# Kernel optimization log

Hardware: AMD Instinct MI355X
Metric: run time of the kernel (lower is better)

The kernel has to match this reference:

```python
import jax, jax.numpy as jnp
import numpy as np

B, T, S, G, D, H, W, CHUNK = 2, 4096, 4096, 64, 1024, 16, 512, 256
HD = D // H


def setup_inputs() -> dict:
    key = jax.random.key(0)
    ks = jax.random.split(key, 16)
    std = 1.0 / np.sqrt(D)
    w = lambda k: jax.random.normal(k, (D, D), jnp.float32) * std
    b = lambda k: jax.random.normal(k, (D,), jnp.float32) * 0.01
    return {
        "query": jax.random.normal(ks[0], (B, T, D), jnp.float32),
        "encoder_out": jax.random.normal(ks[1], (B, S, D), jnp.float32),
        "global_tokens": jax.random.normal(ks[2], (B, G, D), jnp.float32),
        "qw": w(ks[3]), "qb": b(ks[4]),
        "kw": w(ks[5]), "kb": b(ks[6]),
        "vw": w(ks[7]), "vb": b(ks[8]),
        "gkw": w(ks[9]), "gkb": b(ks[10]),
        "gvw": w(ks[11]), "gvb": b(ks[12]),
        "ow": w(ks[13]), "ob": b(ks[14]),
        "compression_ratio": 1,
    }


def reference(query, encoder_out, global_tokens, qw, qb, kw, kb, vw, vb,
              gkw, gkb, gvw, gvb, ow, ob, compression_ratio):
    scale = jnp.float32(np.sqrt(HD))
    r = jnp.float32(compression_ratio)
    # expected raw position for each decoder step, clamped to valid src range
    expected = jnp.clip((jnp.arange(T, dtype=jnp.float32) / r).astype(jnp.int32), 0, S - 1)
    expected = jnp.broadcast_to(expected[None], (B, T))  # [B,T]

    lin = lambda x, wt, bs: x @ wt.T + bs  # torch nn.Linear: y = x W^T + b
    q = lin(query, qw, qb).reshape(B, T, H, HD).transpose(0, 2, 1, 3)            # [B,H,T,HD]
    gk = lin(global_tokens, gkw, gkb).reshape(B, G, H, HD).transpose(0, 2, 1, 3)  # [B,H,G,HD]
    gv = lin(global_tokens, gvw, gvb).reshape(B, G, H, HD).transpose(0, 2, 1, 3)
    ak = lin(encoder_out, kw, kb).reshape(B, S, H, HD).transpose(0, 2, 1, 3)      # [B,H,S,HD]
    av = lin(encoder_out, vw, vb).reshape(B, S, H, HD).transpose(0, 2, 1, 3)

    nC = T // CHUNK
    # per-(batch,chunk) window start, from the middle query's expected position
    centers = expected.reshape(B, nC, CHUNK)[:, :, CHUNK // 2]   # [B,nC]
    win_start = jnp.clip(centers - W // 2, 0, S - W)             # [B,nC]; window always full length W
    idx = win_start[:, :, None] + jnp.arange(W)[None, None, :]   # [B,nC,W]

    gather = lambda kv_b, idx_b: kv_b[:, idx_b, :]               # [H,S,HD],[nC,W] -> [H,nC,W,HD]
    wk = jax.vmap(gather)(ak, idx)                               # [B,H,nC,W,HD]
    wv = jax.vmap(gather)(av, idx)

    qc = q.reshape(B, H, nC, CHUNK, HD)
    sg = jnp.einsum('bhcqd,bhgd->bhcqg', qc, gk) / scale          # global scores  [B,H,nC,CHUNK,G]
    sl = jnp.einsum('bhcqd,bhcwd->bhcqw', qc, wk) / scale         # windowed scores [B,H,nC,CHUNK,W]
    attn = jax.nn.softmax(jnp.concatenate([sg, sl], axis=-1), axis=-1)
    out = (jnp.einsum('bhcqg,bhgd->bhcqd', attn[..., :G], gv)
           + jnp.einsum('bhcqw,bhcwd->bhcqd', attn[..., G:], wv))  # [B,H,nC,CHUNK,HD]
    out = out.reshape(B, H, T, HD).transpose(0, 2, 1, 3).reshape(B, T, D)
    return lin(out, ow, ob)
```

## Files before the change

kernel.cpp:

```cpp
#include <hip/hip_runtime.h>

typedef unsigned short u16;
typedef unsigned int u32;
typedef __attribute__((ext_vector_type(4))) float f32x4;
typedef __attribute__((ext_vector_type(16))) float f32x16;
typedef __attribute__((ext_vector_type(8))) short bf16x8;

constexpr int B_ = 2, T_ = 4096, S_ = 4096, G_ = 64, D_ = 1024, H_ = 16, W_ = 512, CHUNK_ = 256;
constexpr int NC_ = T_ / CHUNK_;
constexpr int NT_ = (G_ + W_) / 32;

__device__ __forceinline__ u16 f2bf(float x) {
  u32 u = __builtin_bit_cast(u32, x);
  return (u16)((u + 0x7FFFu + ((u >> 16) & 1u)) >> 16);
}

__global__ __launch_bounds__(256) void cvt_all_kernel(const float* __restrict__ q, const float* __restrict__ e,
                                                      const float* __restrict__ g, const float* __restrict__ w0,
                                                      const float* __restrict__ w1, const float* __restrict__ w2,
                                                      const float* __restrict__ w3, const float* __restrict__ w4,
                                                      const float* __restrict__ w5, u16* __restrict__ dst) {
  int blk = blockIdx.x;
  const float* src;
  int sblk;
  if (blk < 8192) { src = q; sblk = 0; }
  else if (blk < 16384) { src = e; sblk = 8192; }
  else if (blk < 16512) { src = g; sblk = 16384; }
  else if (blk < 17536) { src = w0; sblk = 16512; }
  else if (blk < 18560) { src = w1; sblk = 17536; }
  else if (blk < 19584) { src = w2; sblk = 18560; }
  else if (blk < 20608) { src = w3; sblk = 19584; }
  else if (blk < 21632) { src = w4; sblk = 20608; }
  else { src = w5; sblk = 21632; }
  int li = (blk - sblk) * 256 + threadIdx.x;
  size_t gi = (size_t)blk * 256 + threadIdx.x;
  float4 v = ((const float4*)src)[li];
  uint2 o;
  o.x = (u32)f2bf(v.x) | ((u32)f2bf(v.y) << 16);
  o.y = (u32)f2bf(v.z) | ((u32)f2bf(v.w) << 16);
  ((uint2*)dst)[gi] = o;
}

__global__ __launch_bounds__(256, 2) void proj_kernel(const u16* __restrict__ ex, const u16* __restrict__ qx,
                                                      const u16* __restrict__ gx, const u16* __restrict__ wgt,
                                                      const float* __restrict__ qb, const float* __restrict__ kbias,
                                                      const float* __restrict__ vbias, const float* __restrict__ gkb,
                                                      const float* __restrict__ gvb, u16* __restrict__ q_bf,
                                                      u16* __restrict__ k_bf, u16* __restrict__ gk_bf) {
  __shared__ char lds[73728];
  constexpr size_t NW = (size_t)D_ * D_;
  constexpr size_t NQs = (size_t)B_ * T_ * D_;
  constexpr size_t NGs = (size_t)B_ * G_ * D_;
  const int tid = threadIdx.x;
  const int lane = tid & 63;
  const int wid = tid >> 6;
  const int wm = wid >> 1, wn = wid & 1;
  const int l15 = lane & 15, kg = lane >> 4;

  const int bid = blockIdx.x;
  const u16 *A, *Bt;
  const float *b1, *b2;
  u16* out;
  int row0, col0, mloc;
  bool scale = false, dual = false;
  size_t dsplit = 0;
  if (bid < 512) {
    row0 = (bid & 31) * 256; col0 = (bid >> 5) * 128; mloc = 256;
    A = ex; Bt = wgt + NW; b1 = kbias; b2 = vbias; out = k_bf; dsplit = NQs; dual = true;
  } else if (bid < 768) {
    int i = bid - 512;
    row0 = (i & 31) * 256; col0 = (i >> 5) * 128; mloc = 256;
    A = qx; Bt = wgt; b1 = qb; b2 = qb; out = q_bf; scale = true;
  } else {
    int i = bid - 768;
    row0 = 0; col0 = i * 128; mloc = 128;
    A = gx; Bt = wgt + 3 * NW; b1 = gkb; b2 = gvb; out = gk_bf; dsplit = NGs; dual = true;
  }
  const float* bp = b1;
  u16* op = out;
  if (dual && col0 >= 1024) { bp = b2 - 1024; op = out + (dsplit - 1024); }

  f32x4 acc[8][4];
#pragma unroll
  for (int i = 0; i < 8; i++)
#pragma unroll
    for (int j = 0; j < 4; j++)
#pragma unroll
      for (int r = 0; r < 4; r++) acc[i][j][r] = 0.f;

  const char* Abase = (const char*)A;
  const char* Bbase = (const char*)Bt;
  const int swb = 16 * ((tid & 3) ^ ((tid >> 3) & 3));

  auto stageA = [&](int slot, int kt) {
#pragma unroll
    for (int p = 0; p < 4; p++) {
      int dst = slot * 16384 + p * 4096 + tid * 16;
      const char* g = Abase + (size_t)(row0 + p * 64 + (tid >> 2)) * 2048 + kt * 64 + swb;
      __builtin_amdgcn_global_load_lds((const __attribute__((address_space(1))) void*)g,
                                       (__attribute__((address_space(3))) void*)(lds + dst), 16, 0, 0);
    }
  };
  auto stageB = [&](int slot, int kt) {
#pragma unroll
    for (int p = 0; p < 2; p++) {
      int dst = 49152 + slot * 8192 + p * 4096 + tid * 16;
      const char* g = Bbase + (size_t)(col0 + p * 64 + (tid >> 2)) * 2048 + kt * 64 + swb;
      __builtin_amdgcn_global_load_lds((const __attribute__((address_space(1))) void*)g,
                                       (__attribute__((address_space(3))) void*)(lds + dst), 16, 0, 0);
    }
  };

  stageA(0, 0); stageB(0, 0);
  stageA(1, 1); stageB(1, 1);
  asm volatile("s_waitcnt vmcnt(6)" ::: "memory");
  __builtin_amdgcn_s_barrier();

  int cur = 0, nx = 2;
  for (int t = 0; t < 32; ++t) {
    const char* Ab = lds + cur * 16384;
    const char* Bb = lds + 49152 + cur * 8192;
    bf16x8 bfv[2], af[4];
#pragma unroll
    for (int ni = 0; ni < 2; ni++) {
      int r = wn * 64 + ni * 16 + l15;
      (void)r;
    }
    bf16x8 bq[4];
#pragma unroll
    for (int ni = 0; ni < 4; ni++) {
      int r = wn * 64 + ni * 16 + l15;
      bq[ni] = *(const bf16x8*)(Bb + ((r * 64 + kg * 16) ^ (((r >> 1) & 3) << 4)));
    }
#pragma unroll
    for (int mi = 0; mi < 4; mi++) {
      int r = wm * 128 + mi * 16 + l15;
      af[mi] = *(const bf16x8*)(Ab + ((r * 64 + kg * 16) ^ (((r >> 1) & 3) << 4)));
    }
    if (t + 2 < 32) stageA(nx, t + 2);
    __builtin_amdgcn_s_barrier();
    __builtin_amdgcn_s_setprio(1);
#pragma unroll
    for (int mi = 0; mi < 4; mi++)
#pragma unroll
      for (int ni = 0; ni < 4; ni++)
        acc[mi][ni] = __builtin_amdgcn_mfma_f32_16x16x32_bf16(bq[ni], af[mi], acc[mi][ni], 0, 0, 0);
    __builtin_amdgcn_s_setprio(0);
    __builtin_amdgcn_s_barrier();
#pragma unroll
    for (int mi = 0; mi < 4; mi++) {
      int r = wm * 128 + (mi + 4) * 16 + l15;
      af[mi] = *(const bf16x8*)(Ab + ((r * 64 + kg * 16) ^ (((r >> 1) & 3) << 4)));
    }
    if (t + 2 < 32) stageB(nx, t + 2);
    __builtin_amdgcn_s_barrier();
    __builtin_amdgcn_s_setprio(1);
#pragma unroll
    for (int mi = 0; mi < 4; mi++)
#pragma unroll
      for (int ni = 0; ni < 4; ni++)
        acc[mi + 4][ni] = __builtin_amdgcn_mfma_f32_16x16x32_bf16(bq[ni], af[mi], acc[mi + 4][ni], 0, 0, 0);
    __builtin_amdgcn_s_setprio(0);
    if (t < 30) {
      asm volatile("s_waitcnt vmcnt(6)" ::: "memory");
    } else if (t == 30) {
      asm volatile("s_waitcnt vmcnt(0)" ::: "memory");
    }
    __builtin_amdgcn_s_barrier();
    cur = cur == 2 ? 0 : cur + 1;
    nx = nx == 2 ? 0 : nx + 1;
  }

  float4 bv4[4];
#pragma unroll
  for (int ni = 0; ni < 4; ni++) bv4[ni] = *(const float4*)&bp[col0 + wn * 64 + ni * 16 + kg * 4];
#pragma unroll
  for (int mi = 0; mi < 8; mi++) {
    int rloc = wm * 128 + mi * 16 + l15;
    if (rloc >= mloc) continue;
    size_t grow = (size_t)(row0 + rloc);
#pragma unroll
    for (int ni = 0; ni < 4; ni++) {
      int gcol = col0 + wn * 64 + ni * 16 + kg * 4;
      float v0 = acc[mi][ni][0] + bv4[ni].x;
      float v1 = acc[mi][ni][1] + bv4[ni].y;
      float v2 = acc[mi][ni][2] + bv4[ni].z;
      float v3 = acc[mi][ni][3] + bv4[ni].w;
      if (scale) {
        v0 *= 0.18033688011112042f; v1 *= 0.18033688011112042f;
        v2 *= 0.18033688011112042f; v3 *= 0.18033688011112042f;
      }
      uint2 o;
      asm("v_cvt_pk_bf16_f32 %0, %1, %2" : "=v"(o.x) : "v"(v0), "v"(v1));
      asm("v_cvt_pk_bf16_f32 %0, %1, %2" : "=v"(o.y) : "v"(v2), "v"(v3));
      *(uint2*)&op[grow * 1024 + gcol] = o;
    }
  }
}

template <int MODE>
__global__ __launch_bounds__(256) void gemm_kernel(const u16* __restrict__ A, const u16* __restrict__ Bt,
                                                   const float* __restrict__ bias, const float* __restrict__ bias2,
                                                   size_t split, void* __restrict__ out) {
  __shared__ char lds[32768];
  char* As = lds;
  char* Bs = lds + 16384;
  const int tid = threadIdx.x;
  const int lane = tid & 63;
  const int wv = tid >> 6;
  const int wr = wv >> 1, wc = wv & 1;
  const int l15 = lane & 15, kg = lane >> 4;
  const int row0 = blockIdx.x * 128;
  const int col0 = blockIdx.y * 128;

  f32x4 acc[4][4];
#pragma unroll
  for (int i = 0; i < 4; i++)
#pragma unroll
    for (int j = 0; j < 4; j++)
#pragma unroll
      for (int r = 0; r < 4; r++) acc[i][j][r] = 0.f;

  const char* Abase = (const char*)A;
  const char* Bbase = (const char*)Bt;

  const int kb = 16 * ((lane & 3) ^ ((lane >> 3) & 3));
  auto stage = [&](int bufsel, int k0) {
#pragma unroll
    for (int c = 0; c < 2; c++) {
      int arow = wv * 32 + c * 16 + (lane >> 2);
      int dsto = bufsel * 8192 + wv * 2048 + c * 1024 + lane * 16;
      const char* ga = Abase + ((size_t)(row0 + arow) * 2048 + (size_t)k0 * 2 + kb);
      __builtin_amdgcn_global_load_lds((const __attribute__((address_space(1))) void*)ga,
                                       (__attribute__((address_space(3))) void*)(As + dsto), 16, 0, 0);
      const char* gb = Bbase + ((size_t)(col0 + arow) * 2048 + (size_t)k0 * 2 + kb);
      __builtin_amdgcn_global_load_lds((const __attribute__((address_space(1))) void*)gb,
                                       (__attribute__((address_space(3))) void*)(Bs + dsto), 16, 0, 0);
    }
  };

  stage(0, 0);
  __syncthreads();

  for (int it = 0; it < 32; ++it) {
    const int cur = it & 1;
    if (it + 1 < 32) stage(cur ^ 1, (it + 1) * 32);

    const char* Ab = As + cur * 8192;
    const char* Bb = Bs + cur * 8192;
    bf16x8 af[4], bfv[4];
#pragma unroll
    for (int mi = 0; mi < 4; mi++) {
      int row = wr * 64 + mi * 16 + l15;
      af[mi] = *(const bf16x8*)(Ab + ((row * 64 + kg * 16) ^ ((row & 6) << 3)));
    }
#pragma unroll
    for (int ni = 0; ni < 4; ni++) {
      int row = wc * 64 + ni * 16 + l15;
      bfv[ni] = *(const bf16x8*)(Bb + ((row * 64 + kg * 16) ^ ((row & 6) << 3)));
    }
    __builtin_amdgcn_s_setprio(1);
#pragma unroll
    for (int mi = 0; mi < 4; mi++)
#pragma unroll
      for (int ni = 0; ni < 4; ni++)
        acc[mi][ni] = __builtin_amdgcn_mfma_f32_16x16x32_bf16(bfv[ni], af[mi], acc[mi][ni], 0, 0, 0);
    __builtin_amdgcn_s_setprio(0);
    __syncthreads();
  }

  const float* bp = bias;
  (void)bias2; (void)split;
  float4 bv4[4];
#pragma unroll
  for (int ni = 0; ni < 4; ni++) bv4[ni] = *(const float4*)&bp[col0 + wc * 64 + ni * 16 + kg * 4];
#pragma unroll
  for (int mi = 0; mi < 4; mi++) {
    size_t grow = (size_t)(row0 + wr * 64 + mi * 16 + l15);
#pragma unroll
    for (int ni = 0; ni < 4; ni++) {
      int gcol = col0 + wc * 64 + ni * 16 + kg * 4;
      float v0 = acc[mi][ni][0] + bv4[ni].x;
      float v1 = acc[mi][ni][1] + bv4[ni].y;
      float v2 = acc[mi][ni][2] + bv4[ni].z;
      float v3 = acc[mi][ni][3] + bv4[ni].w;
      if (MODE == 2) {
        float4 fo = {v0, v1, v2, v3};
        *(float4*)&((float*)out)[grow * 1024 + gcol] = fo;
      } else {
        uint2 o;
        asm("v_cvt_pk_bf16_f32 %0, %1, %2" : "=v"(o.x) : "v"(v0), "v"(v1));
        asm("v_cvt_pk_bf16_f32 %0, %1, %2" : "=v"(o.y) : "v"(v2), "v"(v3));
        *(uint2*)&((u16*)out)[grow * 1024 + gcol] = o;
      }
    }
  }
}

__global__ __launch_bounds__(512, 4) void attn_kernel(const u16* __restrict__ q_bf, const u16* __restrict__ k_bf,
                                                      const u16* __restrict__ v_bf, const u16* __restrict__ gk_bf,
                                                      const u16* __restrict__ gv_bf, u16* __restrict__ ao,
                                                      const int* __restrict__ rptr) {
  __shared__ u16 smem[16384];
  const int c = blockIdx.x, h = blockIdx.y, b = blockIdx.z;
  const int tid = threadIdx.x;
  const int lane = tid & 63, wv = tid >> 6;
  const int l31 = lane & 31, half = lane >> 5;
  const int t0 = c * CHUNK_;

  int rr = rptr[0];
  int centert = c * CHUNK_ + CHUNK_ / 2;
  int expected = (int)((float)centert / (float)rr);
  expected = min(max(expected, 0), S_ - 1);
  int ws0 = min(max(expected - W_ / 2, 0), S_ - W_);

  bf16x8 qf[4];
  {
    const u16* qrow = q_bf + ((size_t)(b * T_ + t0 + wv * 32 + l31)) * D_ + h * 64 + half * 8;
#pragma unroll
    for (int s = 0; s < 4; s++) qf[s] = *(const bf16x8*)(qrow + s * 16);
  }

  const int skey = (tid & 255) >> 3, shq = tid & 7;
  const bool isK = tid < 256;

  auto load_tile = [&](int j) -> uint4 {
    const u16* base;
    size_t row;
    if (j < 2) {
      base = isK ? gk_bf : gv_bf;
      row = (size_t)(b * G_ + j * 32 + skey);
    } else {
      base = isK ? k_bf : v_bf;
      row = (size_t)(b * S_ + ws0 + (j - 2) * 32 + skey);
    }
    return *(const uint4*)(base + row * D_ + h * 64 + shq * 8);
  };

  f32x16 oacc[2];
#pragma unroll
  for (int i = 0; i < 2; i++)
#pragma unroll
    for (int r = 0; r < 16; r++) oacc[i][r] = 0.f;
  float mrun = -1e30f, lsum = 0.f;

  uint4 stg = load_tile(0);

  for (int j = 0; j < NT_; j++) {
    const int bsel = j & 1;
    if (isK) {
      *(uint4*)((char*)smem + bsel * 4096 + ((skey * 128 + shq * 16) ^ ((skey & 7) << 4))) = stg;
    } else {
      const u16* pv = (const u16*)&stg;
      char* bp = (char*)smem + 8192 + bsel * 5248 + shq * 656 + skey * 2;
#pragma unroll
      for (int e = 0; e < 8; e++) *(u16*)(bp + e * 80) = pv[e];
    }
    if (j + 1 < NT_) stg = load_tile(j + 1);
    __syncthreads();

    const int kbase = bsel * 4096;
    const int vtb = 8192 + bsel * 5248;

    f32x16 sacc;
#pragma unroll
    for (int r = 0; r < 16; r++) sacc[r] = 0.f;
    __builtin_amdgcn_s_setprio(1);
#pragma unroll
    for (int s = 0; s < 4; s++) {
      int kbx = kbase + ((l31 * 128 + half * 16 + s * 32) ^ ((l31 & 7) << 4));
      bf16x8 kf = *(const bf16x8*)((char*)smem + kbx);
      sacc = __builtin_amdgcn_mfma_f32_32x32x16_bf16(kf, qf[s], sacc, 0, 0, 0);
    }
    __builtin_amdgcn_s_setprio(0);

    float t0m = fmaxf(fmaxf(sacc[0], sacc[1]), sacc[2]);
    float t1m = fmaxf(fmaxf(sacc[3], sacc[4]), sacc[5]);
    float t2m = fmaxf(fmaxf(sacc[6], sacc[7]), sacc[8]);
    float t3m = fmaxf(fmaxf(sacc[9], sacc[10]), sacc[11]);
    float t4m = fmaxf(fmaxf(sacc[12], sacc[13]), sacc[14]);
    float tmax = fmaxf(fmaxf(fmaxf(t0m, t1m), fmaxf(t2m, t3m)), fmaxf(t4m, sacc[15]));
    tmax = fmaxf(tmax, __shfl_xor(tmax, 32));
    if (__any(tmax > mrun + 8.f)) {
      float mnew = fmaxf(mrun, tmax);
      float fac = __builtin_amdgcn_exp2f(mrun - mnew);
      mrun = mnew;
      lsum *= fac;
#pragma unroll
      for (int i = 0; i < 2; i++)
#pragma unroll
        for (int r = 0; r < 16; r++) oacc[i][r] *= fac;
    }
    float p[16];
#pragma unroll
    for (int r = 0; r < 16; r++) p[r] = __builtin_amdgcn_exp2f(sacc[r] - mrun);
    float s0s = (p[0] + p[1]) + (p[2] + p[3]);
    float s1s = (p[4] + p[5]) + (p[6] + p[7]);
    float s2s = (p[8] + p[9]) + (p[10] + p[11]);
    float s3s = (p[12] + p[13]) + (p[14] + p[15]);
    float tsum = (s0s + s1s) + (s2s + s3s);
    tsum += __shfl_xor(tsum, 32);
    lsum += tsum;

    u32 xs[8], px[8];
#pragma unroll
    for (int i = 0; i < 8; i++)
      asm("v_cvt_pk_bf16_f32 %0, %1, %2" : "=v"(xs[i]) : "v"(p[2 * i]), "v"(p[2 * i + 1]));
#pragma unroll
    for (int i = 0; i < 8; i++) px[i] = (u32)__shfl_xor((int)xs[i], 32);
    u32 Bk[2][4];
    Bk[0][0] = half ? px[2] : xs[0];
    Bk[0][1] = half ? px[3] : xs[1];
    Bk[0][2] = half ? xs[2] : px[0];
    Bk[0][3] = half ? xs[3] : px[1];
    Bk[1][0] = half ? px[6] : xs[4];
    Bk[1][1] = half ? px[7] : xs[5];
    Bk[1][2] = half ? xs[6] : px[4];
    Bk[1][3] = half ? xs[7] : px[5];

    int vro = vtb + l31 * 80 + ((l31 >> 3) << 4) + half * 16;
    __builtin_amdgcn_s_setprio(1);
#pragma unroll
    for (int hdf = 0; hdf < 2; hdf++) {
#pragma unroll
      for (int ks = 0; ks < 2; ks++) {
        bf16x8 vf = *(const bf16x8*)((const char*)smem + vro + hdf * 2624 + ks * 32);
        uint4 u4;
        u4.x = Bk[ks][0]; u4.y = Bk[ks][1]; u4.z = Bk[ks][2]; u4.w = Bk[ks][3];
        bf16x8 pb = __builtin_bit_cast(bf16x8, u4);
        oacc[hdf] = __builtin_amdgcn_mfma_f32_32x32x16_bf16(vf, pb, oacc[hdf], 0, 0, 0);
      }
    }
    __builtin_amdgcn_s_setprio(0);
  }

  __syncthreads();
  float inv = 1.f / lsum;
#pragma unroll
  for (int hdf = 0; hdf < 2; hdf++) {
#pragma unroll
    for (int a = 0; a < 4; a++) {
      float f0 = oacc[hdf][4 * a] * inv, f1 = oacc[hdf][4 * a + 1] * inv;
      float f2 = oacc[hdf][4 * a + 2] * inv, f3 = oacc[hdf][4 * a + 3] * inv;
      uint2 o;
      asm("v_cvt_pk_bf16_f32 %0, %1, %2" : "=v"(o.x) : "v"(f0), "v"(f1));
      asm("v_cvt_pk_bf16_f32 %0, %1, %2" : "=v"(o.y) : "v"(f2), "v"(f3));
      int off = wv * 4096 + l31 * 128 + ((16 * a + 8 * half + 64 * hdf) ^ ((l31 & 7) << 4));
      *(uint2*)((char*)smem + off) = o;
    }
  }
  __syncthreads();
#pragma unroll
  for (int it = 0; it < 4; it++) {
    int byteo = (tid + it * 512) * 16;
    int row = byteo >> 7;
    int colb = byteo & 127;
    uint4 vv = *(const uint4*)((const char*)smem + row * 128 + (colb ^ ((row & 7) << 4)));
    *(uint4*)(ao + ((size_t)(b * T_ + t0 + row)) * D_ + h * 64 + (colb >> 1)) = vv;
  }
}

extern "C" void kernel_launch(void* const* d_in, const int* in_sizes, int n_in,
                              void* d_out, int out_size, void* d_ws, size_t ws_size,
                              hipStream_t stream) {
  (void)in_sizes; (void)n_in; (void)out_size; (void)ws_size;
  const float* query = (const float*)d_in[0];
  const float* enc = (const float*)d_in[1];
  const float* glob = (const float*)d_in[2];
  const float* qw = (const float*)d_in[3];
  const float* qb = (const float*)d_in[4];
  const float* kw = (const float*)d_in[5];
  const float* kb = (const float*)d_in[6];
  const float* vw = (const float*)d_in[7];
  const float* vb = (const float*)d_in[8];
  const float* gkw = (const float*)d_in[9];
  const float* gkb = (const float*)d_in[10];
  const float* gvw = (const float*)d_in[11];
  const float* gvb = (const float*)d_in[12];
  const float* ow = (const float*)d_in[13];
  const float* ob = (const float*)d_in[14];
  const int* rp = (const int*)d_in[15];

  const size_t NQ = (size_t)B_ * T_ * D_;
  const size_t NG = (size_t)B_ * G_ * D_;
  const size_t NW = (size_t)D_ * D_;

  u16* ws = (u16*)d_ws;
  u16* qx = ws;
  u16* ex = qx + NQ;
  u16* gx = ex + NQ;
  u16* wgt = gx + NG;
  u16* q_bf = wgt + 6 * NW;
  u16* k_bf = q_bf + NQ;
  u16* v_bf = k_bf + NQ;
  u16* gk_bf = v_bf + NQ;
  u16* gv_bf = gk_bf + NG;
  u16* ao = gv_bf + NG;

  cvt_all_kernel<<<22656, 256, 0, stream>>>(query, enc, glob, qw, kw, vw, gkw, gvw, ow, ws);

  proj_kernel<<<784, 256, 0, stream>>>(ex, qx, gx, wgt, qb, kb, vb, gkb, gvb, q_bf, k_bf, gk_bf);

  attn_kernel<<<dim3(NC_, H_, B_), 512, 0, stream>>>(q_bf, k_bf, v_bf, gk_bf, gv_bf, ao, rp);

  gemm_kernel<2><<<dim3(64, 8), 256, 0, stream>>>(ao, wgt + 5 * NW, ob, ob, 0, d_out);
}
```

Before: 151.6 us.

## Load projection B operand directly into registers, drop its LDS staging

The projection GEMM used to stage the weight (B) tile through LDS alongside A. It now loads each wave's B fragments straight from global memory into registers, double-buffered across iterations, while A stays triple-buffered in LDS. This shrinks LDS from 72KB to 48KB per block, which may allow more resident blocks, and cuts barriers per k-step from three to one. In exchange, B rows are reloaded redundantly by waves sharing a column (no reuse across wm), and vmcnt accounting now mixes register and LDS-direct loads.

```diff
diff --git a/kernel.cpp b/kernel.cpp
--- a/kernel.cpp
+++ b/kernel.cpp
@@ -47,7 +47,7 @@
                                                       const float* __restrict__ vbias, const float* __restrict__ gkb,
                                                       const float* __restrict__ gvb, u16* __restrict__ q_bf,
                                                       u16* __restrict__ k_bf, u16* __restrict__ gk_bf) {
-  __shared__ char lds[73728];
+  __shared__ char lds[49152];
   constexpr size_t NW = (size_t)D_ * D_;
   constexpr size_t NQs = (size_t)B_ * T_ * D_;
   constexpr size_t NGs = (size_t)B_ * G_ * D_;
@@ -101,44 +101,41 @@
                                        (__attribute__((address_space(3))) void*)(lds + dst), 16, 0, 0);
     }
   };
-  auto stageB = [&](int slot, int kt) {
-#pragma unroll
-    for (int p = 0; p < 2; p++) {
-      int dst = 49152 + slot * 8192 + p * 4096 + tid * 16;
-      const char* g = Bbase + (size_t)(col0 + p * 64 + (tid >> 2)) * 2048 + kt * 64 + swb;
-      __builtin_amdgcn_global_load_lds((const __attribute__((address_space(1))) void*)g,
-                                       (__attribute__((address_space(3))) void*)(lds + dst), 16, 0, 0);
-    }
-  };
-
-  stageA(0, 0); stageB(0, 0);
-  stageA(1, 1); stageB(1, 1);
-  asm volatile("s_waitcnt vmcnt(6)" ::: "memory");
-  __builtin_amdgcn_s_barrier();
-
-  int cur = 0, nx = 2;
-  for (int t = 0; t < 32; ++t) {
-    const char* Ab = lds + cur * 16384;
-    const char* Bb = lds + 49152 + cur * 8192;
-    bf16x8 bfv[2], af[4];
-#pragma unroll
-    for (int ni = 0; ni < 2; ni++) {
-      int r = wn * 64 + ni * 16 + l15;
-      (void)r;
-    }
+
+  const char* bptr[4];
+#pragma unroll
+  for (int ni = 0; ni < 4; ni++)
+    bptr[ni] = Bbase + (size_t)(col0 + wn * 64 + ni * 16 + l15) * 2048 + kg * 16;
+
+  uint4 bA[4], bB[4];
+#pragma unroll
+  for (int ni = 0; ni < 4; ni++) bA[ni] = *(const uint4*)(bptr[ni]);
+  stageA(0, 0);
+  stageA(1, 1);
+
+  auto tile = [&](int t, uint4* bc, uint4* bn) {
+    if (t + 1 < 32) {
+#pragma unroll
+      for (int ni = 0; ni < 4; ni++) bn[ni] = *(const uint4*)(bptr[ni] + (size_t)(t + 1) * 64);
+    }
+    if (t < 31) {
+      asm volatile("s_waitcnt vmcnt(8)" ::: "memory");
+    } else {
+      asm volatile("s_waitcnt vmcnt(0)" ::: "memory");
+    }
+    __builtin_amdgcn_s_barrier();
+    if (t + 2 < 32) stageA((t + 2) % 3, t + 2);
+
+    const char* Ab = lds + (t % 3) * 16384;
     bf16x8 bq[4];
 #pragma unroll
-    for (int ni = 0; ni < 4; ni++) {
-      int r = wn * 64 + ni * 16 + l15;
-      bq[ni] = *(const bf16x8*)(Bb + ((r * 64 + kg * 16) ^ (((r >> 1) & 3) << 4)));
-    }
+    for (int ni = 0; ni < 4; ni++) bq[ni] = __builtin_bit_cast(bf16x8, bc[ni]);
+    bf16x8 af[4];
 #pragma unroll
     for (int mi = 0; mi < 4; mi++) {
       int r = wm * 128 + mi * 16 + l15;
       af[mi] = *(const bf16x8*)(Ab + ((r * 64 + kg * 16) ^ (((r >> 1) & 3) << 4)));
     }
-    if (t + 2 < 32) stageA(nx, t + 2);
-    __builtin_amdgcn_s_barrier();
     __builtin_amdgcn_s_setprio(1);
 #pragma unroll
     for (int mi = 0; mi < 4; mi++)
@@ -146,14 +143,11 @@
       for (int ni = 0; ni < 4; ni++)
         acc[mi][ni] = __builtin_amdgcn_mfma_f32_16x16x32_bf16(bq[ni], af[mi], acc[mi][ni], 0, 0, 0);
     __builtin_amdgcn_s_setprio(0);
-    __builtin_amdgcn_s_barrier();
 #pragma unroll
     for (int mi = 0; mi < 4; mi++) {
       int r = wm * 128 + (mi + 4) * 16 + l15;
       af[mi] = *(const bf16x8*)(Ab + ((r * 64 + kg * 16) ^ (((r >> 1) & 3) << 4)));
     }
-    if (t + 2 < 32) stageB(nx, t + 2);
-    __builtin_amdgcn_s_barrier();
     __builtin_amdgcn_s_setprio(1);
 #pragma unroll
     for (int mi = 0; mi < 4; mi++)
@@ -161,14 +155,11 @@
       for (int ni = 0; ni < 4; ni++)
         acc[mi + 4][ni] = __builtin_amdgcn_mfma_f32_16x16x32_bf16(bq[ni], af[mi], acc[mi + 4][ni], 0, 0, 0);
     __builtin_amdgcn_s_setprio(0);
-    if (t < 30) {
-      asm volatile("s_waitcnt vmcnt(6)" ::: "memory");
-    } else if (t == 30) {
-      asm volatile("s_waitcnt vmcnt(0)" ::: "memory");
-    }
-    __builtin_amdgcn_s_barrier();
-    cur = cur == 2 ? 0 : cur + 1;
-    nx = nx == 2 ? 0 : nx + 1;
+  };
+
+  for (int tt = 0; tt < 32; tt += 2) {
+    tile(tt, bA, bB);
+    tile(tt + 1, bB, bA);
   }
 
   float4 bv4[4];
```

After: 183.6 us. +21.1%, slower.

## Rewrite output projection GEMM with 256x128 tiles and triple-buffered LDS pipeline

Applied to the files above, without the earlier changes.

Replaces the 128x128 double-buffered output projection GEMM with a 256x128 tile kernel that uses three LDS stages, split A/B staging interleaved with the MFMA halves, and explicit vmcnt waits. It mirrors the structure already used in the projection kernel. Each block does more work per operand load and keeps loads further ahead of compute. The grid shrinks from 512 to 256 blocks, which may leave parts of the GPU idle, and LDS use per block grows. It also drops some dead code in the projection kernel.

```diff
diff --git a/kernel.cpp b/kernel.cpp
--- a/kernel.cpp
+++ b/kernel.cpp
@@ -120,12 +120,7 @@
   for (int t = 0; t < 32; ++t) {
     const char* Ab = lds + cur * 16384;
     const char* Bb = lds + 49152 + cur * 8192;
-    bf16x8 bfv[2], af[4];
-#pragma unroll
-    for (int ni = 0; ni < 2; ni++) {
-      int r = wn * 64 + ni * 16 + l15;
-      (void)r;
-    }
+    bf16x8 af[4];
     bf16x8 bq[4];
 #pragma unroll
     for (int ni = 0; ni < 4; ni++) {
@@ -198,24 +193,22 @@
   }
 }
 
-template <int MODE>
-__global__ __launch_bounds__(256) void gemm_kernel(const u16* __restrict__ A, const u16* __restrict__ Bt,
-                                                   const float* __restrict__ bias, const float* __restrict__ bias2,
-                                                   size_t split, void* __restrict__ out) {
-  __shared__ char lds[32768];
-  char* As = lds;
-  char* Bs = lds + 16384;
+__global__ __launch_bounds__(256, 2) void gemmO_kernel(const u16* __restrict__ A, const u16* __restrict__ Bt,
+                                                       const float* __restrict__ bias, float* __restrict__ out) {
+  __shared__ char lds[73728];
   const int tid = threadIdx.x;
   const int lane = tid & 63;
-  const int wv = tid >> 6;
-  const int wr = wv >> 1, wc = wv & 1;
+  const int wid = tid >> 6;
+  const int wm = wid >> 1, wn = wid & 1;
   const int l15 = lane & 15, kg = lane >> 4;
-  const int row0 = blockIdx.x * 128;
-  const int col0 = blockIdx.y * 128;
-
-  f32x4 acc[4][4];
-#pragma unroll
-  for (int i = 0; i < 4; i++)
+
+  const int bid = blockIdx.x;
+  const int row0 = (bid & 31) * 256;
+  const int col0 = (bid >> 5) * 128;
+
+  f32x4 acc[8][4];
+#pragma unroll
+  for (int i = 0; i < 8; i++)
 #pragma unroll
     for (int j = 0; j < 4; j++)
 #pragma unroll
@@ -223,76 +216,97 @@
 
   const char* Abase = (const char*)A;
   const char* Bbase = (const char*)Bt;
-
-  const int kb = 16 * ((lane & 3) ^ ((lane >> 3) & 3));
-  auto stage = [&](int bufsel, int k0) {
-#pragma unroll
-    for (int c = 0; c < 2; c++) {
-      int arow = wv * 32 + c * 16 + (lane >> 2);
-      int dsto = bufsel * 8192 + wv * 2048 + c * 1024 + lane * 16;
-      const char* ga = Abase + ((size_t)(row0 + arow) * 2048 + (size_t)k0 * 2 + kb);
-      __builtin_amdgcn_global_load_lds((const __attribute__((address_space(1))) void*)ga,
-                                       (__attribute__((address_space(3))) void*)(As + dsto), 16, 0, 0);
-      const char* gb = Bbase + ((size_t)(col0 + arow) * 2048 + (size_t)k0 * 2 + kb);
-      __builtin_amdgcn_global_load_lds((const __attribute__((address_space(1))) void*)gb,
-                                       (__attribute__((address_space(3))) void*)(Bs + dsto), 16, 0, 0);
+  const int swb = 16 * ((tid & 3) ^ ((tid >> 3) & 3));
+
+  auto stageA = [&](int slot, int kt) {
+#pragma unroll
+    for (int p = 0; p < 4; p++) {
+      int dst = slot * 16384 + p * 4096 + tid * 16;
+      const char* g = Abase + (size_t)(row0 + p * 64 + (tid >> 2)) * 2048 + kt * 64 + swb;
+      __builtin_amdgcn_global_load_lds((const __attribute__((address_space(1))) void*)g,
+                                       (__attribute__((address_space(3))) void*)(lds + dst), 16, 0, 0);
     }
   };
-
-  stage(0, 0);
-  __syncthreads();
-
-  for (int it = 0; it < 32; ++it) {
-    const int cur = it & 1;
-    if (it + 1 < 32) stage(cur ^ 1, (it + 1) * 32);
-
-    const char* Ab = As + cur * 8192;
-    const char* Bb = Bs + cur * 8192;
-    bf16x8 af[4], bfv[4];
+  auto stageB = [&](int slot, int kt) {
+#pragma unroll
+    for (int p = 0; p < 2; p++) {
+      int dst = 49152 + slot * 8192 + p * 4096 + tid * 16;
+      const char* g = Bbase + (size_t)(col0 + p * 64 + (tid >> 2)) * 2048 + kt * 64 + swb;
+      __builtin_amdgcn_global_load_lds((const __attribute__((address_space(1))) void*)g,
+                                       (__attribute__((address_space(3))) void*)(lds + dst), 16, 0, 0);
+    }
+  };
+
+  stageA(0, 0); stageB(0, 0);
+  stageA(1, 1); stageB(1, 1);
+  asm volatile("s_waitcnt vmcnt(6)" ::: "memory");
+  __builtin_amdgcn_s_barrier();
+
+  int cur = 0, nx = 2;
+  for (int t = 0; t < 32; ++t) {
+    const char* Ab = lds + cur * 16384;
+    const char* Bb = lds + 49152 + cur * 8192;
+    bf16x8 af[4];
+    bf16x8 bq[4];
+#pragma unroll
+    for (int ni = 0; ni < 4; ni++) {
+      int r = wn * 64 + ni * 16 + l15;
+      bq[ni] = *(const bf16x8*)(Bb + ((r * 64 + kg * 16) ^ (((r >> 1) & 3) << 4)));
+    }
 #pragma unroll
     for (int mi = 0; mi < 4; mi++) {
-      int row = wr * 64 + mi * 16 + l15;
-      af[mi] = *(const bf16x8*)(Ab + ((row * 64 + kg * 16) ^ ((row & 6) << 3)));
-    }
+      int r = wm * 128 + mi * 16 + l15;
+      af[mi] = *(const bf16x8*)(Ab + ((r * 64 + kg * 16) ^ (((r >> 1) & 3) << 4)));
+    }
+    if (t + 2 < 32) stageA(nx, t + 2);
+    __builtin_amdgcn_s_barrier();
+    __builtin_amdgcn_s_setprio(1);
+#pragma unroll
+    for (int mi = 0; mi < 4; mi++)
+#pragma unroll
+      for (int ni = 0; ni < 4; ni++)
+        acc[mi][ni] = __builtin_amdgcn_mfma_f32_16x16x32_bf16(bq[ni], af[mi], acc[mi][ni], 0, 0, 0);
+    __builtin_amdgcn_s_setprio(0);
+    __builtin_amdgcn_s_barrier();
+#pragma unroll
+    for (int mi = 0; mi < 4; mi++) {
+      int r = wm * 128 + (mi + 4) * 16 + l15;
+      af[mi] = *(const bf16x8*)(Ab + ((r * 64 + kg * 16) ^ (((r >> 1) & 3) << 4)));
+    }
+    if (t + 2 < 32) stageB(nx, t + 2);
+    __builtin_amdgcn_s_barrier();
+    __builtin_amdgcn_s_setprio(1);
+#pragma unroll
+    for (int mi = 0; mi < 4; mi++)
+#pragma unroll
+      for (int ni = 0; ni < 4; ni++)
+        acc[mi + 4][ni] = __builtin_amdgcn_mfma_f32_16x16x32_bf16(bq[ni], af[mi], acc[mi + 4][ni], 0, 0, 0);
+    __builtin_amdgcn_s_setprio(0);
+    if (t < 30) {
+      asm volatile("s_waitcnt vmcnt(6)" ::: "memory");
+    } else if (t == 30) {
+      asm volatile("s_waitcnt vmcnt(0)" ::: "memory");
+    }
+    __builtin_amdgcn_s_barrier();
+    cur = cur == 2 ? 0 : cur + 1;
+    nx = nx == 2 ? 0 : nx + 1;
+  }
+
+  float4 bv4[4];
+#pragma unroll
+  for (int ni = 0; ni < 4; ni++) bv4[ni] = *(const float4*)&bias[col0 + wn * 64 + ni * 16 + kg * 4];
+#pragma unroll
+  for (int mi = 0; mi < 8; mi++) {
+    size_t grow = (size_t)(row0 + wm * 128 + mi * 16 + l15);
 #pragma unroll
     for (int ni = 0; ni < 4; ni++) {
-      int row = wc * 64 + ni * 16 + l15;
-      bfv[ni] = *(const bf16x8*)(Bb + ((row * 64 + kg * 16) ^ ((row & 6) << 3)));
-    }
-    __builtin_amdgcn_s_setprio(1);
-#pragma unroll
-    for (int mi = 0; mi < 4; mi++)
-#pragma unroll
-      for (int ni = 0; ni < 4; ni++)
-        acc[mi][ni] = __builtin_amdgcn_mfma_f32_16x16x32_bf16(bfv[ni], af[mi], acc[mi][ni], 0, 0, 0);
-    __builtin_amdgcn_s_setprio(0);
-    __syncthreads();
-  }
-
-  const float* bp = bias;
-  (void)bias2; (void)split;
-  float4 bv4[4];
-#pragma unroll
-  for (int ni = 0; ni < 4; ni++) bv4[ni] = *(const float4*)&bp[col0 + wc * 64 + ni * 16 + kg * 4];
-#pragma unroll
-  for (int mi = 0; mi < 4; mi++) {
-    size_t grow = (size_t)(row0 + wr * 64 + mi * 16 + l15);
-#pragma unroll
-    for (int ni = 0; ni < 4; ni++) {
-      int gcol = col0 + wc * 64 + ni * 16 + kg * 4;
-      float v0 = acc[mi][ni][0] + bv4[ni].x;
-      float v1 = acc[mi][ni][1] + bv4[ni].y;
-      float v2 = acc[mi][ni][2] + bv4[ni].z;
-      float v3 = acc[mi][ni][3] + bv4[ni].w;
-      if (MODE == 2) {
-        float4 fo = {v0, v1, v2, v3};
-        *(float4*)&((float*)out)[grow * 1024 + gcol] = fo;
-      } else {
-        uint2 o;
-        asm("v_cvt_pk_bf16_f32 %0, %1, %2" : "=v"(o.x) : "v"(v0), "v"(v1));
-        asm("v_cvt_pk_bf16_f32 %0, %1, %2" : "=v"(o.y) : "v"(v2), "v"(v3));
-        *(uint2*)&((u16*)out)[grow * 1024 + gcol] = o;
-      }
+      int gcol = col0 + wn * 64 + ni * 16 + kg * 4;
+      float4 fo;
+      fo.x = acc[mi][ni][0] + bv4[ni].x;
+      fo.y = acc[mi][ni][1] + bv4[ni].y;
+      fo.z = acc[mi][ni][2] + bv4[ni].z;
+      fo.w = acc[mi][ni][3] + bv4[ni].w;
+      *(float4*)&out[grow * 1024 + gcol] = fo;
     }
   }
 }
@@ -503,5 +517,5 @@
 
   attn_kernel<<<dim3(NC_, H_, B_), 512, 0, stream>>>(q_bf, k_bf, v_bf, gk_bf, gv_bf, ao, rp);
 
-  gemm_kernel<2><<<dim3(64, 8), 256, 0, stream>>>(ao, wgt + 5 * NW, ob, ob, 0, d_out);
+  gemmO_kernel<<<256, 256, 0, stream>>>(ao, wgt + 5 * NW, ob, (float*)d_out);
 }
```

After: 151.8 us. About the same (+0.1%).
